# Optimization experiments

Measured on AMD Instinct MI355X. Metric: run time of the kernel, lower is better.

The kernel has to match this reference:

```python
import jax, jax.numpy as jnp
import numpy as np

B, L = 4, 1024
D_IN, D_MODEL = 2, 512
N_LAYERS, D_STATE, D_CONV, EXPAND, DT_RANK = 2, 16, 4, 2, 32
D_INNER = EXPAND * D_MODEL
EPS = 1e-5


def setup_inputs() -> dict:
    key = jax.random.key(0)
    ks = jax.random.split(key, 10)
    s = 0.02
    return {
        "x": jax.random.normal(ks[0], (B, L, D_IN), jnp.float32),
        "emb_W": jax.random.normal(ks[1], (D_MODEL, D_IN), jnp.float32) * s,
        "emb_b": jnp.zeros((D_MODEL,), jnp.float32),
        "norm_w": jnp.ones((N_LAYERS, D_MODEL), jnp.float32),
        "in_proj_W": jax.random.normal(ks[2], (N_LAYERS, 2 * D_INNER, D_MODEL), jnp.float32) * s,
        "conv_W": jax.random.normal(ks[3], (N_LAYERS, D_INNER, 1, D_CONV), jnp.float32) * s,
        "conv_b": jnp.zeros((N_LAYERS, D_INNER), jnp.float32),
        "x_proj_W": jax.random.normal(ks[4], (N_LAYERS, DT_RANK + 2 * D_STATE, D_INNER), jnp.float32) * s,
        "dt_proj_W": jax.random.normal(ks[5], (N_LAYERS, D_INNER, DT_RANK), jnp.float32) * s,
        "dt_proj_b": jax.random.uniform(ks[6], (N_LAYERS, D_INNER), jnp.float32, -4.0, -2.0),
        "A_log": jnp.log(jnp.broadcast_to(jnp.arange(1, D_STATE + 1, dtype=jnp.float32), (N_LAYERS, D_INNER, D_STATE)) + 0.0),
        "Dskip": jnp.ones((N_LAYERS, D_INNER), jnp.float32),
        "out_proj_W": jax.random.normal(ks[7], (N_LAYERS, D_MODEL, D_INNER), jnp.float32) * s,
        "normf_w": jnp.ones((D_MODEL,), jnp.float32),
    }


def rmsnorm(x, w):
    return x * jax.lax.rsqrt(jnp.mean(x * x, axis=-1, keepdims=True) + EPS) * w


def selective_scan(u, delta, A, Bm, Cm, Dskip):
    # u, delta: (B,L,ED); A: (ED,N); Bm, Cm: (B,L,N); Dskip: (ED,)
    deltaA = jnp.exp(delta[..., None] * A)                      # (B,L,ED,N)
    BX = (delta[..., None] * Bm[:, :, None, :]) * u[..., None]  # (B,L,ED,N)

    def step(h, inp):
        dA, bx, c = inp
        h = dA * h + bx                       # (B,ED,N)
        y = jnp.einsum('ben,bn->be', h, c)    # (B,ED)
        return h, y

    h0 = jnp.zeros((u.shape[0], u.shape[2], A.shape[1]), u.dtype)
    _, ys = jax.lax.scan(step, h0, (deltaA.swapaxes(0, 1), BX.swapaxes(0, 1), Cm.swapaxes(0, 1)))
    y = ys.swapaxes(0, 1)                     # (B,L,ED)
    return y + Dskip * u


def mamba_layer(x, norm_w, ipW, cW, cb, xpW, dtW, dtb, A_log, Dk, opW):
    h = rmsnorm(x, norm_w)
    xz = h @ ipW.T                            # (B,L,2*ED)
    u, z = jnp.split(xz, 2, axis=-1)
    # causal depthwise conv over sequence dim
    uc = jax.lax.conv_general_dilated(
        u.swapaxes(1, 2), cW, window_strides=(1,), padding=[(D_CONV - 1, 0)],
        feature_group_count=D_INNER, dimension_numbers=('NCH', 'OIH', 'NCH'))
    u = jax.nn.silu(uc.swapaxes(1, 2) + cb)   # (B,L,ED)
    xdb = u @ xpW.T                           # (B,L,dt_rank+2N)
    dt, Bm, Cm = jnp.split(xdb, [DT_RANK, DT_RANK + D_STATE], axis=-1)
    delta = jax.nn.softplus(dt @ dtW.T + dtb)
    A = -jnp.exp(A_log)
    y = selective_scan(u, delta, A, Bm, Cm, Dk)
    y = y * jax.nn.silu(z)
    return x + y @ opW.T


def reference(x, emb_W, emb_b, norm_w, in_proj_W, conv_W, conv_b, x_proj_W,
              dt_proj_W, dt_proj_b, A_log, Dskip, out_proj_W, normf_w):
    h = x @ emb_W.T + emb_b                   # (B,L,D_MODEL)
    for l in range(N_LAYERS):
        h = mamba_layer(h, norm_w[l], in_proj_W[l], conv_W[l], conv_b[l],
                        x_proj_W[l], dt_proj_W[l], dt_proj_b[l], A_log[l],
                        Dskip[l], out_proj_W[l])
    return rmsnorm(h, normf_w)
```

## Files before the change

### kernel.cpp

```cpp
#include <hip/hip_runtime.h>
#include <math.h>
#include <stddef.h>

#define BB 4
#define LL 1024
#define DM 512
#define ED 1024
#define NST 16
#define DTR 32
#define XDBC 64
#define BL (BB*LL)
#define CS 16
#define NC 64
#define LDSK 40
#define XKS 16
#define XPAD 68
#define DPAD 132

typedef __attribute__((ext_vector_type(8))) short bf16x8;
typedef __attribute__((ext_vector_type(4))) float f32x4;
typedef unsigned short ushort_t;

__device__ __forceinline__ float silu_f(float x) { return x / (1.f + __expf(-x)); }

__device__ __forceinline__ ushort_t f2b(float f) {
    unsigned int u = __float_as_uint(f);
    unsigned int r = (u + 0x7FFFu + ((u >> 16) & 1u)) >> 16;
    return (ushort_t)r;
}
__device__ __forceinline__ float b2f(ushort_t v) {
    return __uint_as_float(((unsigned int)v) << 16);
}
__device__ __forceinline__ ushort_t f2h(float f) {
    _Float16 h = (_Float16)f;
    return *(ushort_t*)&h;
}
__device__ __forceinline__ float h2f(ushort_t v) {
    _Float16 h = *(_Float16*)&v;
    return (float)h;
}

__global__ void k_embed(const float* __restrict__ x, const float* __restrict__ W,
                        const float* __restrict__ bias, float* __restrict__ h) {
    int i = blockIdx.x * 256 + threadIdx.x;
    if (i >= BL * DM) return;
    int d = i % DM, r = i / DM;
    h[i] = x[r * 2 + 0] * W[d * 2 + 0] + x[r * 2 + 1] * W[d * 2 + 1] + bias[d];
}

__global__ void k_cvt(const float* __restrict__ in, ushort_t* __restrict__ out, int n4) {
    int i = blockIdx.x * 256 + threadIdx.x;
    if (i >= n4) return;
    float4 v = *(const float4*)(in + (size_t)i * 4);
    ushort_t o[4] = {f2b(v.x), f2b(v.y), f2b(v.z), f2b(v.w)};
    *(uint2*)(out + (size_t)i * 4) = *(uint2*)o;
}

template <int BF16OUT>
__global__ __launch_bounds__(256) void k_rmsnorm(const float* __restrict__ in,
                                                 const float* __restrict__ w,
                                                 void* __restrict__ outp) {
    int m = blockIdx.x;
    int tid = threadIdx.x;
    const float* row = in + (size_t)m * DM;
    float2 v = *(const float2*)(row + tid * 2);
    float ss = v.x * v.x + v.y * v.y;
    #pragma unroll
    for (int o = 32; o > 0; o >>= 1) ss += __shfl_down(ss, o, 64);
    __shared__ float red[4];
    int wid = tid >> 6;
    if ((tid & 63) == 0) red[wid] = ss;
    __syncthreads();
    float tot = red[0] + red[1] + red[2] + red[3];
    float rs = rsqrtf(tot * (1.f / DM) + 1e-5f);
    float2 wv = *(const float2*)(w + tid * 2);
    float ox = v.x * rs * wv.x;
    float oy = v.y * rs * wv.y;
    if (BF16OUT) {
        ushort_t o[2] = {f2b(ox), f2b(oy)};
        *(unsigned int*)((ushort_t*)outp + (size_t)m * DM + tid * 2) = *(unsigned int*)o;
    } else {
        *(float2*)((float*)outp + (size_t)m * DM + tid * 2) = make_float2(ox, oy);
    }
}

template <int ADDRES, int BF16OUT>
__global__ __launch_bounds__(256) void k_bgemm(const ushort_t* __restrict__ A,
                                               const ushort_t* __restrict__ W,
                                               const float* __restrict__ Res,
                                               void* __restrict__ C,
                                               int M, int N, int K, int lda, int ldc) {
    __shared__ ushort_t As[128 * LDSK];
    __shared__ ushort_t Bs[128 * LDSK];
    int tid = threadIdx.x;
    int bm = blockIdx.y * 128, bn = blockIdx.x * 128;
    int wave = tid >> 6, lane = tid & 63;
    int wr = wave >> 1, wc = wave & 1;
    int lr = lane & 15, lk = (lane >> 4) * 8;
    int srow = tid >> 2;
    int skb = (tid & 3) * 8;
    f32x4 acc[4][4];
    #pragma unroll
    for (int i = 0; i < 4; ++i)
        #pragma unroll
        for (int j = 0; j < 4; ++j) acc[i][j] = (f32x4){0.f, 0.f, 0.f, 0.f};

    for (int k0 = 0; k0 < K; k0 += 32) {
        uint4 a0 = *(const uint4*)(A + (size_t)(bm + srow) * lda + k0 + skb);
        uint4 a1 = *(const uint4*)(A + (size_t)(bm + 64 + srow) * lda + k0 + skb);
        uint4 b0 = *(const uint4*)(W + (size_t)(bn + srow) * K + k0 + skb);
        uint4 b1 = *(const uint4*)(W + (size_t)(bn + 64 + srow) * K + k0 + skb);
        __syncthreads();
        *(uint4*)(As + srow * LDSK + skb) = a0;
        *(uint4*)(As + (64 + srow) * LDSK + skb) = a1;
        *(uint4*)(Bs + srow * LDSK + skb) = b0;
        *(uint4*)(Bs + (64 + srow) * LDSK + skb) = b1;
        __syncthreads();
        bf16x8 af[4], bfr[4];
        #pragma unroll
        for (int i = 0; i < 4; ++i)
            af[i] = *(const bf16x8*)(As + (wr * 64 + i * 16 + lr) * LDSK + lk);
        #pragma unroll
        for (int j = 0; j < 4; ++j)
            bfr[j] = *(const bf16x8*)(Bs + (wc * 64 + j * 16 + lr) * LDSK + lk);
        #pragma unroll
        for (int i = 0; i < 4; ++i)
            #pragma unroll
            for (int j = 0; j < 4; ++j)
                acc[i][j] = __builtin_amdgcn_mfma_f32_16x16x32_bf16(af[i], bfr[j], acc[i][j], 0, 0, 0);
    }
    int crow0 = bm + wr * 64 + (lane >> 4) * 4;
    int ccol0 = bn + wc * 64 + lr;
    #pragma unroll
    for (int i = 0; i < 4; ++i)
        #pragma unroll
        for (int j = 0; j < 4; ++j)
            #pragma unroll
            for (int r = 0; r < 4; ++r) {
                size_t off = (size_t)(crow0 + i * 16 + r) * ldc + ccol0 + j * 16;
                float v = acc[i][j][r];
                if (ADDRES) v += Res[off];
                if (BF16OUT) ((ushort_t*)C)[off] = f2b(v);
                else         ((float*)C)[off] = v;
            }
}

__global__ __launch_bounds__(256) void k_xproj(const float* __restrict__ A,
                                               const float* __restrict__ W,
                                               float* __restrict__ Pp) {
    __shared__ float As[64][XPAD];
    __shared__ float Ws[64][XPAD];
    int tid = threadIdx.x;
    int k0 = blockIdx.x * 64;
    int bm = blockIdx.y * 64;
    int r = tid >> 2;
    int kc = (tid & 3) * 16;
    const float4* ap = (const float4*)(A + (size_t)(bm + r) * ED + k0 + kc);
    const float4* wp = (const float4*)(W + (size_t)r * ED + k0 + kc);
    #pragma unroll
    for (int i = 0; i < 4; ++i) {
        float4 av = ap[i];
        float4 wv = wp[i];
        As[kc + i * 4 + 0][r] = av.x; As[kc + i * 4 + 1][r] = av.y;
        As[kc + i * 4 + 2][r] = av.z; As[kc + i * 4 + 3][r] = av.w;
        Ws[kc + i * 4 + 0][r] = wv.x; Ws[kc + i * 4 + 1][r] = wv.y;
        Ws[kc + i * 4 + 2][r] = wv.z; Ws[kc + i * 4 + 3][r] = wv.w;
    }
    __syncthreads();
    int tm = (tid >> 4) * 4;
    int tn = (tid & 15) * 4;
    float acc[4][4] = {};
    #pragma unroll 4
    for (int k = 0; k < 64; ++k) {
        float4 a = *(const float4*)&As[k][tm];
        float4 b = *(const float4*)&Ws[k][tn];
        acc[0][0] += a.x * b.x; acc[0][1] += a.x * b.y; acc[0][2] += a.x * b.z; acc[0][3] += a.x * b.w;
        acc[1][0] += a.y * b.x; acc[1][1] += a.y * b.y; acc[1][2] += a.y * b.z; acc[1][3] += a.y * b.w;
        acc[2][0] += a.z * b.x; acc[2][1] += a.z * b.y; acc[2][2] += a.z * b.z; acc[2][3] += a.z * b.w;
        acc[3][0] += a.w * b.x; acc[3][1] += a.w * b.y; acc[3][2] += a.w * b.z; acc[3][3] += a.w * b.w;
    }
    float* pp = Pp + (size_t)blockIdx.x * BL * XDBC;
    #pragma unroll
    for (int i = 0; i < 4; ++i)
        *(float4*)(pp + (size_t)(bm + tm + i) * XDBC + tn) =
            make_float4(acc[i][0], acc[i][1], acc[i][2], acc[i][3]);
}

__global__ void k_xred(const float* __restrict__ Pp, float* __restrict__ xdb) {
    int i = blockIdx.x * 256 + threadIdx.x;
    float4 s = make_float4(0.f, 0.f, 0.f, 0.f);
    #pragma unroll
    for (int sl = 0; sl < XKS; ++sl) {
        float4 v = *(const float4*)(Pp + (size_t)sl * BL * XDBC + (size_t)i * 4);
        s.x += v.x; s.y += v.y; s.z += v.z; s.w += v.w;
    }
    *(float4*)(xdb + (size_t)i * 4) = s;
}

__global__ void k_conv(const ushort_t* __restrict__ xzb, const float* __restrict__ cw,
                       const float* __restrict__ cb, float* __restrict__ u) {
    int i = blockIdx.x * 256 + threadIdx.x;
    if (i >= BL * ED) return;
    int e = i % ED;
    int t = (i / ED) % LL;
    int b = i / (ED * LL);
    const ushort_t* col = xzb + (size_t)b * LL * 2048 + e;
    float4 w4 = *(const float4*)(cw + e * 4);
    float acc = cb[e];
    if (t >= 3) acc += b2f(col[(size_t)(t - 3) * 2048]) * w4.x;
    if (t >= 2) acc += b2f(col[(size_t)(t - 2) * 2048]) * w4.y;
    if (t >= 1) acc += b2f(col[(size_t)(t - 1) * 2048]) * w4.z;
    acc += b2f(col[(size_t)t * 2048]) * w4.w;
    u[i] = silu_f(acc);
}

__global__ __launch_bounds__(256) void k_delta(const float* __restrict__ xdb,
                                               const float* __restrict__ dtW,
                                               const float* __restrict__ dtb,
                                               ushort_t* __restrict__ dyh) {
    __shared__ float Dt[32][DPAD];
    __shared__ float Wt[32][DPAD];
    int tid = threadIdx.x;
    int bm = blockIdx.y * 128;
    int bn = blockIdx.x * 128;
    int r = tid >> 1;
    int hh = (tid & 1) * 16;
    const float4* dp = (const float4*)(xdb + (size_t)(bm + r) * XDBC + hh);
    const float4* wp = (const float4*)(dtW + (size_t)(bn + r) * 32 + hh);
    #pragma unroll
    for (int i = 0; i < 4; ++i) {
        float4 v = dp[i];
        Dt[hh + i * 4 + 0][r] = v.x; Dt[hh + i * 4 + 1][r] = v.y;
        Dt[hh + i * 4 + 2][r] = v.z; Dt[hh + i * 4 + 3][r] = v.w;
        float4 w = wp[i];
        Wt[hh + i * 4 + 0][r] = w.x; Wt[hh + i * 4 + 1][r] = w.y;
        Wt[hh + i * 4 + 2][r] = w.z; Wt[hh + i * 4 + 3][r] = w.w;
    }
    __syncthreads();
    int tm = (tid >> 4) * 8;
    int tn = (tid & 15) * 8;
    float acc[8][8] = {};
    #pragma unroll 8
    for (int k = 0; k < 32; ++k) {
        float4 a0 = *(const float4*)&Dt[k][tm];
        float4 a1 = *(const float4*)&Dt[k][tm + 4];
        float4 b0 = *(const float4*)&Wt[k][tn];
        float4 b1 = *(const float4*)&Wt[k][tn + 4];
        float a[8] = {a0.x, a0.y, a0.z, a0.w, a1.x, a1.y, a1.z, a1.w};
        float b[8] = {b0.x, b0.y, b0.z, b0.w, b1.x, b1.y, b1.z, b1.w};
        #pragma unroll
        for (int i = 0; i < 8; ++i)
            #pragma unroll
            for (int j = 0; j < 8; ++j) acc[i][j] += a[i] * b[j];
    }
    float4 t0 = *(const float4*)(dtb + bn + tn);
    float4 t1 = *(const float4*)(dtb + bn + tn + 4);
    float bias[8] = {t0.x, t0.y, t0.z, t0.w, t1.x, t1.y, t1.z, t1.w};
    #pragma unroll
    for (int i = 0; i < 8; ++i) {
        ushort_t o16[8];
        #pragma unroll
        for (int j = 0; j < 8; ++j) {
            float v = acc[i][j] + bias[j];
            v = (v > 20.f) ? v : __logf(1.f + __expf(v));
            o16[j] = f2h(v);
        }
        size_t off = (size_t)(bm + tm + i) * ED + bn + tn;
        *(uint4*)(dyh + off) = *(uint4*)o16;
    }
}

__global__ __launch_bounds__(256) void k_scan1(const ushort_t* __restrict__ dyh,
                                               const float* __restrict__ u,
                                               const float* __restrict__ xdb,
                                               const float* __restrict__ A_log,
                                               float* __restrict__ P,
                                               float* __restrict__ S) {
    int tid = threadIdx.x;
    int e = ((blockIdx.x & 3) << 8) + tid;
    int c = (blockIdx.x >> 2) & (NC - 1);
    int b = blockIdx.x >> 8;
    float Ac[16];
    const float4* ap = (const float4*)(A_log + (size_t)e * NST);
    #pragma unroll
    for (int q = 0; q < 4; ++q) {
        float4 a = ap[q];
        Ac[q * 4 + 0] = -__expf(a.x); Ac[q * 4 + 1] = -__expf(a.y);
        Ac[q * 4 + 2] = -__expf(a.z); Ac[q * 4 + 3] = -__expf(a.w);
    }
    float h[16] = {};
    float s = 0.f;
    const ushort_t* dp = dyh + ((size_t)b * LL + c * CS) * ED + e;
    const float* up = u + ((size_t)b * LL + c * CS) * ED + e;
    const float* xp = xdb + ((size_t)b * LL + c * CS) * XDBC;
    for (int tt = 0; tt < CS; ++tt) {
        float dv = h2f(dp[(size_t)tt * ED]);
        float uv = up[(size_t)tt * ED];
        s += dv;
        float du = dv * uv;
        const float4* bp = (const float4*)(xp + tt * XDBC + DTR);
        #pragma unroll
        for (int q = 0; q < 4; ++q) {
            float4 bv = bp[q];
            h[q * 4 + 0] = __expf(dv * Ac[q * 4 + 0]) * h[q * 4 + 0] + du * bv.x;
            h[q * 4 + 1] = __expf(dv * Ac[q * 4 + 1]) * h[q * 4 + 1] + du * bv.y;
            h[q * 4 + 2] = __expf(dv * Ac[q * 4 + 2]) * h[q * 4 + 2] + du * bv.z;
            h[q * 4 + 3] = __expf(dv * Ac[q * 4 + 3]) * h[q * 4 + 3] + du * bv.w;
        }
    }
    float4* pp = (float4*)(P + ((size_t)(b * NC + c) * ED + e) * NST);
    pp[0] = make_float4(h[0], h[1], h[2], h[3]);
    pp[1] = make_float4(h[4], h[5], h[6], h[7]);
    pp[2] = make_float4(h[8], h[9], h[10], h[11]);
    pp[3] = make_float4(h[12], h[13], h[14], h[15]);
    S[(size_t)(b * NC + c) * ED + e] = s;
}

__global__ __launch_bounds__(256) void k_scan2(float* __restrict__ P,
                                               const float* __restrict__ S,
                                               const float* __restrict__ A_log) {
    int i = blockIdx.x * 256 + threadIdx.x;
    int n = i & 15;
    int e = (i >> 4) & (ED - 1);
    int b = i >> 14;
    float Ac = -__expf(A_log[(size_t)e * NST + n]);
    float hin = 0.f;
    for (int c = 0; c < NC; ++c) {
        size_t base = (size_t)(b * NC + c) * ED + e;
        float p = P[base * NST + n];
        float s = S[base];
        P[base * NST + n] = hin;
        hin = __expf(Ac * s) * hin + p;
    }
}

__global__ __launch_bounds__(256) void k_scan3(const ushort_t* __restrict__ dyh,
                                               const float* __restrict__ u,
                                               const float* __restrict__ xdb,
                                               const ushort_t* __restrict__ xzb,
                                               const float* __restrict__ A_log,
                                               const float* __restrict__ Dskip,
                                               const float* __restrict__ P,
                                               ushort_t* __restrict__ yb) {
    int tid = threadIdx.x;
    int e = ((blockIdx.x & 3) << 8) + tid;
    int c = (blockIdx.x >> 2) & (NC - 1);
    int b = blockIdx.x >> 8;
    float Ac[16], h[16];
    const float4* ap = (const float4*)(A_log + (size_t)e * NST);
    #pragma unroll
    for (int q = 0; q < 4; ++q) {
        float4 a = ap[q];
        Ac[q * 4 + 0] = -__expf(a.x); Ac[q * 4 + 1] = -__expf(a.y);
        Ac[q * 4 + 2] = -__expf(a.z); Ac[q * 4 + 3] = -__expf(a.w);
    }
    const float4* pp = (const float4*)(P + ((size_t)(b * NC + c) * ED + e) * NST);
    #pragma unroll
    for (int q = 0; q < 4; ++q) {
        float4 hv = pp[q];
        h[q * 4 + 0] = hv.x; h[q * 4 + 1] = hv.y;
        h[q * 4 + 2] = hv.z; h[q * 4 + 3] = hv.w;
    }
    float Dk = Dskip[e];
    const ushort_t* dp = dyh + ((size_t)b * LL + c * CS) * ED + e;
    const float* up = u + ((size_t)b * LL + c * CS) * ED + e;
    const float* xp = xdb + ((size_t)b * LL + c * CS) * XDBC;
    const ushort_t* zp = xzb + ((size_t)b * LL + c * CS) * 2048 + 1024 + e;
    ushort_t* yp = yb + ((size_t)b * LL + c * CS) * ED + e;
    for (int tt = 0; tt < CS; ++tt) {
        float dv = h2f(dp[(size_t)tt * ED]);
        float uv = up[(size_t)tt * ED];
        float zv = b2f(zp[(size_t)tt * 2048]);
        float du = dv * uv;
        const float4* bp = (const float4*)(xp + tt * XDBC + DTR);
        const float4* cp = (const float4*)(xp + tt * XDBC + DTR + NST);
        float y = 0.f;
        #pragma unroll
        for (int q = 0; q < 4; ++q) {
            float4 bv = bp[q];
            float4 cv = cp[q];
            h[q * 4 + 0] = __expf(dv * Ac[q * 4 + 0]) * h[q * 4 + 0] + du * bv.x;
            h[q * 4 + 1] = __expf(dv * Ac[q * 4 + 1]) * h[q * 4 + 1] + du * bv.y;
            h[q * 4 + 2] = __expf(dv * Ac[q * 4 + 2]) * h[q * 4 + 2] + du * bv.z;
            h[q * 4 + 3] = __expf(dv * Ac[q * 4 + 3]) * h[q * 4 + 3] + du * bv.w;
            y += h[q * 4 + 0] * cv.x + h[q * 4 + 1] * cv.y +
                 h[q * 4 + 2] * cv.z + h[q * 4 + 3] * cv.w;
        }
        yp[(size_t)tt * ED] = f2b((y + Dk * uv) * silu_f(zv));
    }
}

extern "C" void kernel_launch(void* const* d_in, const int* in_sizes, int n_in,
                              void* d_out, int out_size, void* d_ws, size_t ws_size,
                              hipStream_t stream) {
    const float* x     = (const float*)d_in[0];
    const float* embW  = (const float*)d_in[1];
    const float* embB  = (const float*)d_in[2];
    const float* normw = (const float*)d_in[3];
    const float* ipW   = (const float*)d_in[4];
    const float* cW    = (const float*)d_in[5];
    const float* cb    = (const float*)d_in[6];
    const float* xpW   = (const float*)d_in[7];
    const float* dtW   = (const float*)d_in[8];
    const float* dtb   = (const float*)d_in[9];
    const float* Alog  = (const float*)d_in[10];
    const float* Dsk   = (const float*)d_in[11];
    const float* opW   = (const float*)d_in[12];
    const float* normfw= (const float*)d_in[13];
    float* out = (float*)d_out;

    float* ws  = (float*)d_ws;
    float* h   = ws;
    ushort_t* xzb = (ushort_t*)(h + (size_t)BL * DM);
    float* u   = (float*)(xzb + (size_t)BL * 2 * ED);
    float* xdb = u + (size_t)BL * ED;
    float* Pp  = xdb + (size_t)BL * XDBC;
    float* S   = Pp + (size_t)BL * ED;
    ushort_t* wip = (ushort_t*)(S + (size_t)BB * NC * ED);
    ushort_t* wop = wip + (size_t)2 * 2 * ED * DM;
    ushort_t* yb  = wop + (size_t)2 * DM * ED;
    float* P      = Pp;
    ushort_t* hnb = (ushort_t*)d_out;
    ushort_t* dyh = (ushort_t*)d_out;

    k_embed<<<(BL * DM + 255) / 256, 256, 0, stream>>>(x, embW, embB, h);
    k_cvt<<<(2 * 2 * ED * DM / 4 + 255) / 256, 256, 0, stream>>>(ipW, wip, 2 * 2 * ED * DM / 4);
    k_cvt<<<(2 * DM * ED / 4 + 255) / 256, 256, 0, stream>>>(opW, wop, 2 * DM * ED / 4);

    for (int l = 0; l < 2; ++l) {
        const float* Al = Alog + (size_t)l * ED * NST;
        k_rmsnorm<1><<<BL, 256, 0, stream>>>(h, normw + (size_t)l * DM, hnb);
        k_bgemm<0, 1><<<dim3(2 * ED / 128, BL / 128), 256, 0, stream>>>(
            hnb, wip + (size_t)l * 2 * ED * DM, nullptr, xzb, BL, 2 * ED, DM, DM, 2 * ED);
        k_conv<<<(BL * ED + 255) / 256, 256, 0, stream>>>(
            xzb, cW + (size_t)l * ED * 4, cb + (size_t)l * ED, u);
        k_xproj<<<dim3(XKS, BL / 64), 256, 0, stream>>>(
            u, xpW + (size_t)l * XDBC * ED, Pp);
        k_xred<<<BL * XDBC / 4 / 256, 256, 0, stream>>>(Pp, xdb);
        k_delta<<<dim3(ED / 128, BL / 128), 256, 0, stream>>>(
            xdb, dtW + (size_t)l * ED * DTR, dtb + (size_t)l * ED, dyh);
        k_scan1<<<BB * NC * (ED / 256), 256, 0, stream>>>(dyh, u, xdb, Al, P, S);
        k_scan2<<<BB * ED * NST / 256, 256, 0, stream>>>(P, S, Al);
        k_scan3<<<BB * NC * (ED / 256), 256, 0, stream>>>(
            dyh, u, xdb, xzb, Al, Dsk + (size_t)l * ED, P, yb);
        k_bgemm<1, 0><<<dim3(DM / 128, BL / 128), 256, 0, stream>>>(
            yb, wop + (size_t)l * DM * ED, h, h, BL, DM, ED, ED, DM);
    }
    k_rmsnorm<0><<<BL, 256, 0, stream>>>(h, normfw, out);
}
```

Baseline: 299.4 us.

## Use direct global-to-LDS loads with swizzle in GEMM, store u as bf16

The bf16 GEMM now loads tiles straight from global memory into LDS with global_load_lds and an XOR-swizzled layout, replacing register staging and padded rows. The out-projection GEMM uses 64-wide N tiles so more blocks are launched. The conv output u is stored as bf16 instead of fp32, which halves its traffic into xproj and both scan kernels, and the two weight-conversion launches are merged into one. Storing u in bf16 lowers its precision, and the GEMM still has no double buffering, so load latency remains exposed.

```diff
diff --git a/kernel.cpp b/kernel.cpp
--- a/kernel.cpp
+++ b/kernel.cpp
@@ -12,7 +12,6 @@
 #define BL (BB*LL)
 #define CS 16
 #define NC 64
-#define LDSK 40
 #define XKS 16
 #define XPAD 68
 #define DPAD 132
@@ -38,6 +37,12 @@
 __device__ __forceinline__ float h2f(ushort_t v) {
     _Float16 h = *(_Float16*)&v;
     return (float)h;
+}
+
+__device__ __forceinline__ void gload16(const ushort_t* g, ushort_t* l) {
+    __builtin_amdgcn_global_load_lds(
+        (const __attribute__((address_space(1))) unsigned int*)g,
+        (__attribute__((address_space(3))) unsigned int*)l, 16, 0, 0);
 }
 
 __global__ void k_embed(const float* __restrict__ x, const float* __restrict__ W,
@@ -48,12 +53,17 @@
     h[i] = x[r * 2 + 0] * W[d * 2 + 0] + x[r * 2 + 1] * W[d * 2 + 1] + bias[d];
 }
 
-__global__ void k_cvt(const float* __restrict__ in, ushort_t* __restrict__ out, int n4) {
+__global__ void k_cvt2(const float* __restrict__ ip, const float* __restrict__ op,
+                       ushort_t* __restrict__ wip, ushort_t* __restrict__ wop,
+                       int n1, int n2) {
     int i = blockIdx.x * 256 + threadIdx.x;
-    if (i >= n4) return;
-    float4 v = *(const float4*)(in + (size_t)i * 4);
+    const float* src; ushort_t* dst; int q;
+    if (i < n1) { src = ip; dst = wip; q = i; }
+    else if (i < n1 + n2) { src = op; dst = wop; q = i - n1; }
+    else return;
+    float4 v = *(const float4*)(src + (size_t)q * 4);
     ushort_t o[4] = {f2b(v.x), f2b(v.y), f2b(v.z), f2b(v.w)};
-    *(uint2*)(out + (size_t)i * 4) = *(uint2*)o;
+    *(uint2*)(dst + (size_t)q * 4) = *(uint2*)o;
 }
 
 template <int BF16OUT>
@@ -84,60 +94,73 @@
     }
 }
 
-template <int ADDRES, int BF16OUT>
+template <int ADDRES, int BF16OUT, int NT>
 __global__ __launch_bounds__(256) void k_bgemm(const ushort_t* __restrict__ A,
                                                const ushort_t* __restrict__ W,
                                                const float* __restrict__ Res,
                                                void* __restrict__ C,
                                                int M, int N, int K, int lda, int ldc) {
-    __shared__ ushort_t As[128 * LDSK];
-    __shared__ ushort_t Bs[128 * LDSK];
-    int tid = threadIdx.x;
-    int bm = blockIdx.y * 128, bn = blockIdx.x * 128;
+    __shared__ ushort_t As[128 * 32];
+    __shared__ ushort_t Bs[NT * 32];
+    constexpr int NFJ = NT / 32;
+    int tid = threadIdx.x;
+    int bm = blockIdx.y * 128, bn = blockIdx.x * NT;
     int wave = tid >> 6, lane = tid & 63;
     int wr = wave >> 1, wc = wave & 1;
-    int lr = lane & 15, lk = (lane >> 4) * 8;
-    int srow = tid >> 2;
-    int skb = (tid & 3) * 8;
-    f32x4 acc[4][4];
+    int lr = lane & 15;
+    int kc = lane >> 4;
+    f32x4 acc[4][NFJ];
     #pragma unroll
     for (int i = 0; i < 4; ++i)
         #pragma unroll
-        for (int j = 0; j < 4; ++j) acc[i][j] = (f32x4){0.f, 0.f, 0.f, 0.f};
+        for (int j = 0; j < NFJ; ++j) acc[i][j] = (f32x4){0.f, 0.f, 0.f, 0.f};
 
     for (int k0 = 0; k0 < K; k0 += 32) {
-        uint4 a0 = *(const uint4*)(A + (size_t)(bm + srow) * lda + k0 + skb);
-        uint4 a1 = *(const uint4*)(A + (size_t)(bm + 64 + srow) * lda + k0 + skb);
-        uint4 b0 = *(const uint4*)(W + (size_t)(bn + srow) * K + k0 + skb);
-        uint4 b1 = *(const uint4*)(W + (size_t)(bn + 64 + srow) * K + k0 + skb);
         __syncthreads();
-        *(uint4*)(As + srow * LDSK + skb) = a0;
-        *(uint4*)(As + (64 + srow) * LDSK + skb) = a1;
-        *(uint4*)(Bs + srow * LDSK + skb) = b0;
-        *(uint4*)(Bs + (64 + srow) * LDSK + skb) = b1;
+        #pragma unroll
+        for (int ii = 0; ii < 2; ++ii) {
+            int g = wave * 128 + ii * 64 + lane;
+            int row = g >> 2;
+            int c = (g & 3) ^ ((g >> 3) & 3);
+            gload16(A + (size_t)(bm + row) * lda + k0 + c * 8,
+                    As + (size_t)(wave * 128 + ii * 64) * 8);
+        }
+        #pragma unroll
+        for (int ii = 0; ii < NFJ / 2; ++ii) {
+            int g = wave * (NFJ / 2) * 64 + ii * 64 + lane;
+            int row = g >> 2;
+            int c = (g & 3) ^ ((g >> 3) & 3);
+            gload16(W + (size_t)(bn + row) * K + k0 + c * 8,
+                    Bs + (size_t)(wave * (NFJ / 2) * 64 + ii * 64) * 8);
+        }
         __syncthreads();
-        bf16x8 af[4], bfr[4];
-        #pragma unroll
-        for (int i = 0; i < 4; ++i)
-            af[i] = *(const bf16x8*)(As + (wr * 64 + i * 16 + lr) * LDSK + lk);
-        #pragma unroll
-        for (int j = 0; j < 4; ++j)
-            bfr[j] = *(const bf16x8*)(Bs + (wc * 64 + j * 16 + lr) * LDSK + lk);
+        bf16x8 af[4], bfr[NFJ];
+        #pragma unroll
+        for (int i = 0; i < 4; ++i) {
+            int ra = wr * 64 + i * 16 + lr;
+            int ca = kc ^ ((ra >> 1) & 3);
+            af[i] = *(const bf16x8*)(As + ra * 32 + ca * 8);
+        }
+        #pragma unroll
+        for (int j = 0; j < NFJ; ++j) {
+            int rb = wc * (NT / 2) + j * 16 + lr;
+            int cb = kc ^ ((rb >> 1) & 3);
+            bfr[j] = *(const bf16x8*)(Bs + rb * 32 + cb * 8);
+        }
         #pragma unroll
         for (int i = 0; i < 4; ++i)
             #pragma unroll
-            for (int j = 0; j < 4; ++j)
+            for (int j = 0; j < NFJ; ++j)
                 acc[i][j] = __builtin_amdgcn_mfma_f32_16x16x32_bf16(af[i], bfr[j], acc[i][j], 0, 0, 0);
     }
     int crow0 = bm + wr * 64 + (lane >> 4) * 4;
-    int ccol0 = bn + wc * 64 + lr;
     #pragma unroll
     for (int i = 0; i < 4; ++i)
         #pragma unroll
-        for (int j = 0; j < 4; ++j)
+        for (int j = 0; j < NFJ; ++j)
             #pragma unroll
             for (int r = 0; r < 4; ++r) {
-                size_t off = (size_t)(crow0 + i * 16 + r) * ldc + ccol0 + j * 16;
+                size_t off = (size_t)(crow0 + i * 16 + r) * ldc + bn + wc * (NT / 2) + j * 16 + lr;
                 float v = acc[i][j][r];
                 if (ADDRES) v += Res[off];
                 if (BF16OUT) ((ushort_t*)C)[off] = f2b(v);
@@ -145,7 +168,7 @@
             }
 }
 
-__global__ __launch_bounds__(256) void k_xproj(const float* __restrict__ A,
+__global__ __launch_bounds__(256) void k_xproj(const ushort_t* __restrict__ A,
                                                const float* __restrict__ W,
                                                float* __restrict__ Pp) {
     __shared__ float As[64][XPAD];
@@ -155,14 +178,20 @@
     int bm = blockIdx.y * 64;
     int r = tid >> 2;
     int kc = (tid & 3) * 16;
-    const float4* ap = (const float4*)(A + (size_t)(bm + r) * ED + k0 + kc);
+    const ushort_t* ap = A + (size_t)(bm + r) * ED + k0 + kc;
     const float4* wp = (const float4*)(W + (size_t)r * ED + k0 + kc);
+    uint4 a0 = *(const uint4*)(ap);
+    uint4 a1 = *(const uint4*)(ap + 8);
+    const ushort_t* pa0 = (const ushort_t*)&a0;
+    const ushort_t* pa1 = (const ushort_t*)&a1;
+    #pragma unroll
+    for (int i = 0; i < 8; ++i) {
+        As[kc + i][r] = b2f(pa0[i]);
+        As[kc + 8 + i][r] = b2f(pa1[i]);
+    }
     #pragma unroll
     for (int i = 0; i < 4; ++i) {
-        float4 av = ap[i];
         float4 wv = wp[i];
-        As[kc + i * 4 + 0][r] = av.x; As[kc + i * 4 + 1][r] = av.y;
-        As[kc + i * 4 + 2][r] = av.z; As[kc + i * 4 + 3][r] = av.w;
         Ws[kc + i * 4 + 0][r] = wv.x; Ws[kc + i * 4 + 1][r] = wv.y;
         Ws[kc + i * 4 + 2][r] = wv.z; Ws[kc + i * 4 + 3][r] = wv.w;
     }
@@ -198,7 +227,7 @@
 }
 
 __global__ void k_conv(const ushort_t* __restrict__ xzb, const float* __restrict__ cw,
-                       const float* __restrict__ cb, float* __restrict__ u) {
+                       const float* __restrict__ cb, ushort_t* __restrict__ u) {
     int i = blockIdx.x * 256 + threadIdx.x;
     if (i >= BL * ED) return;
     int e = i % ED;
@@ -211,7 +240,7 @@
     if (t >= 2) acc += b2f(col[(size_t)(t - 2) * 2048]) * w4.y;
     if (t >= 1) acc += b2f(col[(size_t)(t - 1) * 2048]) * w4.z;
     acc += b2f(col[(size_t)t * 2048]) * w4.w;
-    u[i] = silu_f(acc);
+    u[i] = f2b(silu_f(acc));
 }
 
 __global__ __launch_bounds__(256) void k_delta(const float* __restrict__ xdb,
@@ -271,7 +300,7 @@
 }
 
 __global__ __launch_bounds__(256) void k_scan1(const ushort_t* __restrict__ dyh,
-                                               const float* __restrict__ u,
+                                               const ushort_t* __restrict__ u,
                                                const float* __restrict__ xdb,
                                                const float* __restrict__ A_log,
                                                float* __restrict__ P,
@@ -291,11 +320,11 @@
     float h[16] = {};
     float s = 0.f;
     const ushort_t* dp = dyh + ((size_t)b * LL + c * CS) * ED + e;
-    const float* up = u + ((size_t)b * LL + c * CS) * ED + e;
+    const ushort_t* up = u + ((size_t)b * LL + c * CS) * ED + e;
     const float* xp = xdb + ((size_t)b * LL + c * CS) * XDBC;
     for (int tt = 0; tt < CS; ++tt) {
         float dv = h2f(dp[(size_t)tt * ED]);
-        float uv = up[(size_t)tt * ED];
+        float uv = b2f(up[(size_t)tt * ED]);
         s += dv;
         float du = dv * uv;
         const float4* bp = (const float4*)(xp + tt * XDBC + DTR);
@@ -335,7 +364,7 @@
 }
 
 __global__ __launch_bounds__(256) void k_scan3(const ushort_t* __restrict__ dyh,
-                                               const float* __restrict__ u,
+                                               const ushort_t* __restrict__ u,
                                                const float* __restrict__ xdb,
                                                const ushort_t* __restrict__ xzb,
                                                const float* __restrict__ A_log,
@@ -363,13 +392,13 @@
     }
     float Dk = Dskip[e];
     const ushort_t* dp = dyh + ((size_t)b * LL + c * CS) * ED + e;
-    const float* up = u + ((size_t)b * LL + c * CS) * ED + e;
+    const ushort_t* up = u + ((size_t)b * LL + c * CS) * ED + e;
     const float* xp = xdb + ((size_t)b * LL + c * CS) * XDBC;
     const ushort_t* zp = xzb + ((size_t)b * LL + c * CS) * 2048 + 1024 + e;
     ushort_t* yp = yb + ((size_t)b * LL + c * CS) * ED + e;
     for (int tt = 0; tt < CS; ++tt) {
         float dv = h2f(dp[(size_t)tt * ED]);
-        float uv = up[(size_t)tt * ED];
+        float uv = b2f(up[(size_t)tt * ED]);
         float zv = b2f(zp[(size_t)tt * 2048]);
         float du = dv * uv;
         const float4* bp = (const float4*)(xp + tt * XDBC + DTR);
@@ -412,10 +441,10 @@
     float* ws  = (float*)d_ws;
     float* h   = ws;
     ushort_t* xzb = (ushort_t*)(h + (size_t)BL * DM);
-    float* u   = (float*)(xzb + (size_t)BL * 2 * ED);
-    float* xdb = u + (size_t)BL * ED;
+    ushort_t* ub  = xzb + (size_t)BL * 2 * ED;
+    float* xdb = (float*)(ub + (size_t)BL * ED);
     float* Pp  = xdb + (size_t)BL * XDBC;
-    float* S   = Pp + (size_t)BL * ED;
+    float* S   = Pp + (size_t)XKS * BL * XDBC;
     ushort_t* wip = (ushort_t*)(S + (size_t)BB * NC * ED);
     ushort_t* wop = wip + (size_t)2 * 2 * ED * DM;
     ushort_t* yb  = wop + (size_t)2 * DM * ED;
@@ -424,26 +453,26 @@
     ushort_t* dyh = (ushort_t*)d_out;
 
     k_embed<<<(BL * DM + 255) / 256, 256, 0, stream>>>(x, embW, embB, h);
-    k_cvt<<<(2 * 2 * ED * DM / 4 + 255) / 256, 256, 0, stream>>>(ipW, wip, 2 * 2 * ED * DM / 4);
-    k_cvt<<<(2 * DM * ED / 4 + 255) / 256, 256, 0, stream>>>(opW, wop, 2 * DM * ED / 4);
+    int n1 = 2 * 2 * ED * DM / 4, n2 = 2 * DM * ED / 4;
+    k_cvt2<<<(n1 + n2 + 255) / 256, 256, 0, stream>>>(ipW, opW, wip, wop, n1, n2);
 
     for (int l = 0; l < 2; ++l) {
         const float* Al = Alog + (size_t)l * ED * NST;
         k_rmsnorm<1><<<BL, 256, 0, stream>>>(h, normw + (size_t)l * DM, hnb);
-        k_bgemm<0, 1><<<dim3(2 * ED / 128, BL / 128), 256, 0, stream>>>(
+        k_bgemm<0, 1, 128><<<dim3(2 * ED / 128, BL / 128), 256, 0, stream>>>(
             hnb, wip + (size_t)l * 2 * ED * DM, nullptr, xzb, BL, 2 * ED, DM, DM, 2 * ED);
         k_conv<<<(BL * ED + 255) / 256, 256, 0, stream>>>(
-            xzb, cW + (size_t)l * ED * 4, cb + (size_t)l * ED, u);
+            xzb, cW + (size_t)l * ED * 4, cb + (size_t)l * ED, ub);
         k_xproj<<<dim3(XKS, BL / 64), 256, 0, stream>>>(
-            u, xpW + (size_t)l * XDBC * ED, Pp);
+            ub, xpW + (size_t)l * XDBC * ED, Pp);
         k_xred<<<BL * XDBC / 4 / 256, 256, 0, stream>>>(Pp, xdb);
         k_delta<<<dim3(ED / 128, BL / 128), 256, 0, stream>>>(
             xdb, dtW + (size_t)l * ED * DTR, dtb + (size_t)l * ED, dyh);
-        k_scan1<<<BB * NC * (ED / 256), 256, 0, stream>>>(dyh, u, xdb, Al, P, S);
+        k_scan1<<<BB * NC * (ED / 256), 256, 0, stream>>>(dyh, ub, xdb, Al, P, S);
         k_scan2<<<BB * ED * NST / 256, 256, 0, stream>>>(P, S, Al);
         k_scan3<<<BB * NC * (ED / 256), 256, 0, stream>>>(
-            dyh, u, xdb, xzb, Al, Dsk + (size_t)l * ED, P, yb);
-        k_bgemm<1, 0><<<dim3(DM / 128, BL / 128), 256, 0, stream>>>(
+            dyh, ub, xdb, xzb, Al, Dsk + (size_t)l * ED, P, yb);
+        k_bgemm<1, 0, 64><<<dim3(DM / 64, BL / 128), 256, 0, stream>>>(
             yb, wop + (size_t)l * DM * ED, h, h, BL, DM, ED, ED, DM);
     }
     k_rmsnorm<0><<<BL, 256, 0, stream>>>(h, normfw, out);
```

Result: no change. 297.3 us (-0.7%).
